# Kernel tuning notes

Measured on AMD Instinct MI355X. Metric: run time of the kernel, lower is better.

Reference implementation:

```python
import jax, jax.numpy as jnp
import numpy as np
from jax import lax

N, C, H, W = 16384, 1, 28, 28
HID = 128
EPS = 1e-5


def setup_inputs() -> dict:
    key = jax.random.key(0)
    ks = jax.random.split(key, 12)
    x = jax.random.normal(ks[0], (N, C, H, W), jnp.float32)
    w1 = jax.random.normal(ks[1], (8, 1, 7, 7), jnp.float32) * 0.05
    g1 = 1.0 + 0.1 * jax.random.normal(ks[2], (8,), jnp.float32)
    b1 = 0.1 * jax.random.normal(ks[3], (8,), jnp.float32)
    w2 = jax.random.normal(ks[4], (10, 8, 5, 5), jnp.float32) * 0.05
    g2 = 1.0 + 0.1 * jax.random.normal(ks[5], (10,), jnp.float32)
    b2 = 0.1 * jax.random.normal(ks[6], (10,), jnp.float32)
    w3 = jax.random.normal(ks[7], (HID, 10, 1, 1), jnp.float32) * 0.05
    g3 = 1.0 + 0.1 * jax.random.normal(ks[8], (HID,), jnp.float32)
    b3 = 0.1 * jax.random.normal(ks[9], (HID,), jnp.float32)
    # original inits fc weight to 0 and bias to identity affine; we add a small
    # random weight so theta varies per sample (exercises the sampler)
    fw = jax.random.normal(ks[10], (6, HID), jnp.float32) * 0.01
    fb = jnp.array([1, 0, 0, 0, 1, 0], jnp.float32)
    return {"x": x, "w1": w1, "g1": g1, "b1": b1, "w2": w2, "g2": g2,
            "b2": b2, "w3": w3, "g3": g3, "b3": b3, "fw": fw, "fb": fb}


def conv2d(x, w):
    return lax.conv_general_dilated(x, w, (1, 1), 'VALID',
                                    dimension_numbers=('NCHW', 'OIHW', 'NCHW'))


def batchnorm(x, g, b):
    m = jnp.mean(x, axis=(0, 2, 3), keepdims=True)
    v = jnp.mean((x - m) ** 2, axis=(0, 2, 3), keepdims=True)
    xh = (x - m) * lax.rsqrt(v + EPS)
    return xh * g[None, :, None, None] + b[None, :, None, None]


def maxpool2(x):
    return lax.reduce_window(x, -jnp.inf, lax.max, (1, 1, 2, 2), (1, 1, 2, 2), 'VALID')


def bilinear_sample(img_nhwc, grid):
    # img_nhwc: [N,H,W,C], grid: [N,H,W,2] normalized coords (x, y) in [-1,1]
    ix = (grid[..., 0] + 1.0) * 0.5 * (W - 1)
    iy = (grid[..., 1] + 1.0) * 0.5 * (H - 1)
    x0f = jnp.floor(ix); y0f = jnp.floor(iy)
    wx = ix - x0f; wy = iy - y0f
    x0 = jnp.clip(x0f.astype(jnp.int32), 0, W - 1)
    x1 = jnp.clip(x0 + 1, 0, W - 1)
    y0 = jnp.clip(y0f.astype(jnp.int32), 0, H - 1)
    y1 = jnp.clip(y0 + 1, 0, H - 1)

    def gather(img, yy, xx):  # img [H,W,C], yy/xx [H,W] -> [H,W,C]
        return img[yy, xx]
    g = jax.vmap(gather)
    v00 = g(img_nhwc, y0, x0)
    v01 = g(img_nhwc, y0, x1)
    v10 = g(img_nhwc, y1, x0)
    v11 = g(img_nhwc, y1, x1)
    wx = wx[..., None]; wy = wy[..., None]
    top = v00 * (1 - wx) + v01 * wx
    bot = v10 * (1 - wx) + v11 * wx
    return top * (1 - wy) + bot * wy


def reference(x, w1, g1, b1, w2, g2, b2, w3, g3, b3, fw, fb):
    # localization network
    xs = jax.nn.relu(maxpool2(batchnorm(conv2d(x, w1), g1, b1)))   # [N,8,11,11]
    xs = jax.nn.relu(maxpool2(batchnorm(conv2d(xs, w2), g2, b2)))  # [N,10,3,3]
    xs = jax.nn.relu(batchnorm(conv2d(xs, w3), g3, b3))            # [N,128,3,3]
    xs = jnp.mean(xs, axis=(2, 3))                                 # avgpool 3x3 -> [N,128]
    theta = (xs @ fw.T + fb).reshape(-1, 2, 3)                     # [N,2,3]
    # affine grid over normalized coords
    lin_x = jnp.linspace(-1.0, 1.0, W)
    lin_y = jnp.linspace(-1.0, 1.0, H)
    gx, gy = jnp.meshgrid(lin_x, lin_y)                            # [H,W]
    base = jnp.stack([gx, gy, jnp.ones_like(gx)], axis=-1)         # [H,W,3]
    grid = jnp.einsum('nij,hwj->nhwi', theta, base)                # [N,H,W,2]
    # sample in NHWC (matches the transpose dance in the torch code)
    out = bilinear_sample(jnp.transpose(x, (0, 2, 3, 1)), grid)
    return jnp.transpose(out, (0, 3, 1, 2))                        # back to NCHW
```

## Files before the change

kernel.cpp:

```cpp
#include <hip/hip_runtime.h>


static constexpr float kEPS = 1e-5f;

#define O_SUM1 0
#define O_SSQ1 8
#define O_SUM2 16
#define O_SSQ2 26
#define O_MOM  36
#define O_W2T  104
#define O_THETA 2112
#define O_E1   100864
#define O_E2   15960576
#define O_E2T  17435136

__global__ __launch_bounds__(256) void k_init(const float* __restrict__ w2,
                                              float* __restrict__ ws){
  int i = blockIdx.x*256 + threadIdx.x;
  if (i < 104) ws[i] = 0.f;
  if (i < 2000){
    int ic = i & 7;
    int r  = i >> 3;
    int kx = r % 5; r /= 5;
    int ky = r % 5; r /= 5;
    int oc = r;
    ws[O_W2T + i] = w2[(oc*8 + ic)*25 + ky*5 + kx];
  }
}

__global__ __launch_bounds__(256) void k_conv1(const float* __restrict__ x,
                                               const float* __restrict__ w1,
                                               const float* __restrict__ g1,
                                               float* __restrict__ ws){
  __shared__ float sw[392];
  const int tid = threadIdx.x;
  for (int i = tid; i < 392; i += 256) sw[i] = w1[i];
  __syncthreads();
  const int gid = blockIdx.x*256 + tid;
  const int ph = gid & 1;
  const int c  = (gid >> 1) & 7;
  const int n  = gid >> 4;
  const float* __restrict__ xs = x + n*784;
  const float* __restrict__ wc = sw + c*49;
  const bool pos = (g1[c] >= 0.f);
  float sum=0.f, ssq=0.f;
  float* __restrict__ outp = ws + O_E1 + n*968 + c;
  const int p0 = ph*6;
  const int p1 = ph ? 11 : 6;
  for (int p=p0; p<p1; p++){
    float cm = 0.f, cn = 0.f;
    #pragma unroll
    for (int h=0; h<2; h++){
      float a0[11], a1[11];
      #pragma unroll
      for (int i=0;i<11;i++){ a0[i]=0.f; a1[i]=0.f; }
      #pragma unroll
      for (int j=0;j<8;j++){
        float in[17];
        const float* __restrict__ rb = xs + (2*p+j)*28 + 11*h;
        if (h==0){
          const float4* __restrict__ rp = (const float4*)rb;
          float4 v0=rp[0], v1=rp[1], v2=rp[2], v3=rp[3];
          in[0]=v0.x; in[1]=v0.y; in[2]=v0.z; in[3]=v0.w;
          in[4]=v1.x; in[5]=v1.y; in[6]=v1.z; in[7]=v1.w;
          in[8]=v2.x; in[9]=v2.y; in[10]=v2.z; in[11]=v2.w;
          in[12]=v3.x; in[13]=v3.y; in[14]=v3.z; in[15]=v3.w;
          in[16]=rb[16];
        } else {
          in[0]=rb[0];
          const float4* __restrict__ rp = (const float4*)(rb+1);
          float4 v0=rp[0], v1=rp[1], v2=rp[2], v3=rp[3];
          in[1]=v0.x; in[2]=v0.y; in[3]=v0.z; in[4]=v0.w;
          in[5]=v1.x; in[6]=v1.y; in[7]=v1.z; in[8]=v1.w;
          in[9]=v2.x; in[10]=v2.y; in[11]=v2.z; in[12]=v2.w;
          in[13]=v3.x; in[14]=v3.y; in[15]=v3.z; in[16]=v3.w;
        }
        if (j < 7){
          #pragma unroll
          for (int kx=0;kx<7;kx++){
            float wv = wc[j*7+kx];
            #pragma unroll
            for (int xo=0;xo<11;xo++) a0[xo] = fmaf(wv, in[xo+kx], a0[xo]);
          }
        }
        if (j >= 1){
          #pragma unroll
          for (int kx=0;kx<7;kx++){
            float wv = wc[(j-1)*7+kx];
            #pragma unroll
            for (int xo=0;xo<11;xo++) a1[xo] = fmaf(wv, in[xo+kx], a1[xo]);
          }
        }
      }
      #pragma unroll
      for (int xo=0;xo<11;xo++){
        sum += a0[xo] + a1[xo];
        ssq = fmaf(a0[xo],a0[xo],ssq);
        ssq = fmaf(a1[xo],a1[xo],ssq);
      }
      if (h==0){
        #pragma unroll
        for (int px=0;px<5;px++){
          float m4 = fmaxf(fmaxf(a0[2*px],a0[2*px+1]), fmaxf(a1[2*px],a1[2*px+1]));
          float n4 = fminf(fminf(a0[2*px],a0[2*px+1]), fminf(a1[2*px],a1[2*px+1]));
          outp[(p*11+px)*8] = pos ? m4 : n4;
        }
        cm = fmaxf(a0[10], a1[10]);
        cn = fminf(a0[10], a1[10]);
      } else {
        float m4 = fmaxf(cm, fmaxf(a0[0],a1[0]));
        float n4 = fminf(cn, fminf(a0[0],a1[0]));
        outp[(p*11+5)*8] = pos ? m4 : n4;
        #pragma unroll
        for (int q=0;q<5;q++){
          int l0 = 1+2*q, l1 = 2+2*q;
          float m4q = fmaxf(fmaxf(a0[l0],a0[l1]), fmaxf(a1[l0],a1[l1]));
          float n4q = fminf(fminf(a0[l0],a0[l1]), fminf(a1[l0],a1[l1]));
          outp[(p*11+6+q)*8] = pos ? m4q : n4q;
        }
      }
    }
  }
  sum += __shfl_xor(sum,1);  ssq += __shfl_xor(ssq,1);
  sum += __shfl_xor(sum,16); ssq += __shfl_xor(ssq,16);
  sum += __shfl_xor(sum,32); ssq += __shfl_xor(ssq,32);
  __shared__ float ls[16];
  if (tid < 16) ls[tid] = 0.f;
  __syncthreads();
  int l = tid & 63;
  if ((l & 0x31) == 0){
    atomicAdd(&ls[l>>1], sum);
    atomicAdd(&ls[8 + (l>>1)], ssq);
  }
  __syncthreads();
  if (tid < 16) atomicAdd(&ws[O_SUM1 + tid], ls[tid]);
}

__global__ __launch_bounds__(256) void k_conv2(float* __restrict__ ws,
                                               const float* __restrict__ g1,
                                               const float* __restrict__ b1,
                                               const float* __restrict__ g2){
  __shared__ float sw2[2160];
  for (int i = threadIdx.x; i < 2000; i += 256){
    int oc_ = i/200, r = i - oc_*200;
    sw2[oc_*216 + r] = ws[O_W2T + i];
  }
  __syncthreads();
  float s1r[8], t1r[8];
  {
    const float invM1 = 1.f/7929856.f;
    #pragma unroll
    for (int c=0;c<8;c++){
      float mean = ws[O_SUM1+c]*invM1;
      float var  = ws[O_SSQ1+c]*invM1 - mean*mean;
      float sc = g1[c]*rsqrtf(var + kEPS);
      s1r[c] = sc; t1r[c] = b1[c] - mean*sc;
    }
  }
  const int blk = blockIdx.x;
  const int half = (blk >= 640) ? 1 : 0;
  const int gid = (blk - half*640)*256 + threadIdx.x;
  const int n = gid/10, oc = gid - 10*n;
  const int r0 = half*4;
  const int nrows = half ? 7 : 8;
  const float* __restrict__ wt = sw2 + oc*216;
  const float* __restrict__ base = ws + O_E1 + n*968;
  float acc[28];
  #pragma unroll
  for (int i=0;i<28;i++) acc[i]=0.f;
  for (int jj=0; jj<nrows; ++jj){
    const int iy = r0 + jj;
    #pragma unroll
    for (int icl=0; icl<2; ++icl){
      float4 in4[11];
      #pragma unroll
      for (int q=0;q<11;q++){
        float4 v = *(const float4*)(base + iy*88 + q*8 + icl*4);
        in4[q].x = fmaxf(fmaf(s1r[icl*4+0], v.x, t1r[icl*4+0]), 0.f);
        in4[q].y = fmaxf(fmaf(s1r[icl*4+1], v.y, t1r[icl*4+1]), 0.f);
        in4[q].z = fmaxf(fmaf(s1r[icl*4+2], v.z, t1r[icl*4+2]), 0.f);
        in4[q].w = fmaxf(fmaf(s1r[icl*4+3], v.w, t1r[icl*4+3]), 0.f);
      }
      #pragma unroll
      for (int ol=0; ol<4; ++ol){
        if (half && ol==3) continue;
        const int ky = jj - ol;
        if (ky < 0 || ky > 4) continue;
        const float* __restrict__ wrow = wt + ky*40 + icl*4;
        #pragma unroll
        for (int kx=0;kx<5;kx++){
          float4 w = *(const float4*)(wrow + kx*8);
          #pragma unroll
          for (int ox=0;ox<7;ox++){
            float a = acc[ol*7+ox];
            a = fmaf(w.x, in4[ox+kx].x, a);
            a = fmaf(w.y, in4[ox+kx].y, a);
            a = fmaf(w.z, in4[ox+kx].z, a);
            a = fmaf(w.w, in4[ox+kx].w, a);
            acc[ol*7+ox] = a;
          }
        }
      }
    }
  }
  {
    const int NV = (half ? 3 : 4)*7;
    float sum=0.f, ssq=0.f;
    #pragma unroll
    for (int i=0;i<28;i++){
      if (i < NV){ float v = acc[i]; sum += v; ssq = fmaf(v,v,ssq); }
    }
    __shared__ float ls[20];
    if (threadIdx.x < 20) ls[threadIdx.x] = 0.f;
    __syncthreads();
    atomicAdd(&ls[oc], sum);
    atomicAdd(&ls[10+oc], ssq);
    __syncthreads();
    if (threadIdx.x < 20) atomicAdd(&ws[O_SUM2 + threadIdx.x], ls[threadIdx.x]);
  }
  {
    const bool pos = (g2[oc] >= 0.f);
    const int npy = half ? 1 : 2;
    #pragma unroll
    for (int pl=0; pl<2; pl++){
      if (pl >= npy) continue;
      const int py = half ? 2 : pl;
      #pragma unroll
      for (int px=0;px<3;px++){
        float v00 = acc[(2*pl)*7   + 2*px], v01 = acc[(2*pl)*7   + 2*px+1];
        float v10 = acc[(2*pl+1)*7 + 2*px], v11 = acc[(2*pl+1)*7 + 2*px+1];
        float m4 = fmaxf(fmaxf(v00,v01), fmaxf(v10,v11));
        float n4 = fminf(fminf(v00,v01), fminf(v10,v11));
        ws[O_E2 + (n*9 + py*3 + px)*10 + oc] = pos ? m4 : n4;
      }
    }
  }
}

__global__ __launch_bounds__(256) void k_pool2fin(float* __restrict__ ws,
                                                  const float* __restrict__ g2,
                                                  const float* __restrict__ b2){
  __shared__ float smom[65];
  const int tid = threadIdx.x;
  if (tid < 65) smom[tid] = 0.f;
  __syncthreads();
  const float invM = 1.f/802816.f;
  const int gid = blockIdx.x*256 + tid;
  const int n = gid/9, p = gid - n*9;
  const float* __restrict__ src = ws + O_E2 + gid*10;
  float xv[10];
  #pragma unroll
  for (int c=0;c<10;c++){
    float mean = ws[O_SUM2+c]*invM;
    float var  = ws[O_SSQ2+c]*invM - mean*mean;
    float sc = g2[c]*rsqrtf(var + kEPS);
    float tc = b2[c] - mean*sc;
    float v = fmaxf(fmaf(sc, src[c], tc), 0.f);
    xv[c] = v;
    ws[O_E2T + (p*10 + c)*16384 + n] = v;
  }
  float mu[10], sm[55];
  #pragma unroll
  for (int i=0;i<10;i++) mu[i] = xv[i];
  #pragma unroll
  for (int i=0;i<10;i++){
    #pragma unroll
    for (int j=i;j<10;j++) sm[i*10 - i*(i-1)/2 + (j-i)] = xv[i]*xv[j];
  }
  #pragma unroll
  for (int off=1; off<64; off<<=1){
    #pragma unroll
    for (int i=0;i<10;i++) mu[i] += __shfl_xor(mu[i], off);
    #pragma unroll
    for (int k=0;k<55;k++) sm[k] += __shfl_xor(sm[k], off);
  }
  if ((tid & 63) == 0){
    #pragma unroll
    for (int i=0;i<10;i++) atomicAdd(&smom[i], mu[i]);
    #pragma unroll
    for (int k=0;k<55;k++) atomicAdd(&smom[10+k], sm[k]);
  }
  __syncthreads();
  if (tid < 65) atomicAdd(&ws[O_MOM + tid], smom[tid]);
}

__global__ __launch_bounds__(64) void k_theta(float* __restrict__ ws,
                                              const float* __restrict__ w3,
                                              const float* __restrict__ g3,
                                              const float* __restrict__ b3,
                                              const float* __restrict__ fw,
                                              const float* __restrict__ fb){
  __shared__ float s3[128], t3[128];
  const int tid = threadIdx.x;
  #pragma unroll
  for (int rep=0; rep<2; rep++){
    const int oc = tid + rep*64;
    const float invM = 1.f/147456.f;
    float mu[10], w[10];
    #pragma unroll
    for (int i=0;i<10;i++) mu[i] = ws[O_MOM+i]*invM;
    #pragma unroll
    for (int i=0;i<10;i++) w[i] = w3[oc*10+i];
    float mean3 = 0.f;
    #pragma unroll
    for (int i=0;i<10;i++) mean3 += w[i]*mu[i];
    float var3 = 0.f;
    #pragma unroll
    for (int i=0;i<10;i++){
      #pragma unroll
      for (int j=i;j<10;j++){
        float Sij = ws[O_MOM+10 + i*10 - i*(i-1)/2 + (j-i)]*invM;
        float cov = Sij - mu[i]*mu[j];
        float coef = (i==j) ? 1.f : 2.f;
        var3 += coef * w[i] * w[j] * cov;
      }
    }
    var3 = fmaxf(var3, 0.f);
    float s = g3[oc]*rsqrtf(var3 + kEPS);
    s3[oc] = s;
    t3[oc] = b3[oc] - mean3*s;
  }
  __syncthreads();
  const int n = blockIdx.x*64 + tid;
  float in[90];
  #pragma unroll
  for (int i=0;i<90;i++) in[i] = ws[O_E2T + i*16384 + n];
  float th[6];
  #pragma unroll
  for (int j=0;j<6;j++) th[j] = fb[j];
  for (int oc=0; oc<128; oc++){
    float s = s3[oc], t = t3[oc];
    float fsum = 0.f;
    #pragma unroll
    for (int p=0;p<9;p++){
      float v = 0.f;
      #pragma unroll
      for (int ic=0;ic<10;ic++) v = fmaf(w3[oc*10+ic], in[p*10+ic], v);
      fsum += fmaxf(fmaf(s,v,t), 0.f);
    }
    float feat = fsum * (1.f/9.f);
    #pragma unroll
    for (int j=0;j<6;j++) th[j] = fmaf(fw[j*128+oc], feat, th[j]);
  }
  float* __restrict__ op = ws + O_THETA + n*6;
  #pragma unroll
  for (int j=0;j<6;j++) op[j] = th[j];
}

__global__ __launch_bounds__(256) void k_sample(const float* __restrict__ x,
                                                const float* __restrict__ ws,
                                                float* __restrict__ out){
  const int n = blockIdx.x;
  __shared__ float sx[784];
  const int tid = threadIdx.x;
  if (tid < 196) ((float4*)sx)[tid] = ((const float4*)(x + n*784))[tid];
  __syncthreads();
  const float* __restrict__ th = ws + O_THETA + n*6;
  const float t0=th[0], t1=th[1], t2=th[2], t3=th[3], t4=th[4], t5=th[5];
  float* __restrict__ op = out + n*784;
  for (int idx=tid; idx<784; idx+=256){
    int h = idx/28;
    int wcol = idx - 28*h;
    float gx = fmaf((float)wcol, 2.f/27.f, -1.f);
    float gy = fmaf((float)h,    2.f/27.f, -1.f);
    float ix = (fmaf(t0,gx,fmaf(t1,gy,t2)) + 1.f)*13.5f;
    float iy = (fmaf(t3,gx,fmaf(t4,gy,t5)) + 1.f)*13.5f;
    float x0f = floorf(ix), y0f = floorf(iy);
    float wx = ix - x0f, wy = iy - y0f;
    int x0 = min(max((int)x0f,0),27); int x1 = min(x0+1,27);
    int y0 = min(max((int)y0f,0),27); int y1 = min(y0+1,27);
    float v00 = sx[y0*28+x0], v01 = sx[y0*28+x1];
    float v10 = sx[y1*28+x0], v11 = sx[y1*28+x1];
    float top = v00*(1.f-wx) + v01*wx;
    float bot = v10*(1.f-wx) + v11*wx;
    op[idx] = top*(1.f-wy) + bot*wy;
  }
}

extern "C" void kernel_launch(void* const* d_in, const int* in_sizes, int n_in,
                              void* d_out, int out_size, void* d_ws, size_t ws_size,
                              hipStream_t stream){
  (void)in_sizes; (void)n_in; (void)out_size; (void)ws_size;
  const float* x  = (const float*)d_in[0];
  const float* w1 = (const float*)d_in[1];
  const float* g1 = (const float*)d_in[2];
  const float* b1 = (const float*)d_in[3];
  const float* w2 = (const float*)d_in[4];
  const float* g2 = (const float*)d_in[5];
  const float* b2 = (const float*)d_in[6];
  const float* w3 = (const float*)d_in[7];
  const float* g3 = (const float*)d_in[8];
  const float* b3 = (const float*)d_in[9];
  const float* fw = (const float*)d_in[10];
  const float* fb = (const float*)d_in[11];
  float* ws  = (float*)d_ws;
  float* out = (float*)d_out;

  hipLaunchKernelGGL(k_init,      dim3(8),     dim3(256), 0, stream, w2, ws);
  hipLaunchKernelGGL(k_conv1,     dim3(1024),  dim3(256), 0, stream, x, w1, g1, ws);
  hipLaunchKernelGGL(k_conv2,     dim3(1280),  dim3(256), 0, stream, ws, g1, b1, g2);
  hipLaunchKernelGGL(k_pool2fin,  dim3(576),   dim3(256), 0, stream, ws, g2, b2);
  hipLaunchKernelGGL(k_theta,     dim3(256),   dim3(64),  0, stream, ws, w3, g3, b3, fw, fb);
  hipLaunchKernelGGL(k_sample,    dim3(16384), dim3(256), 0, stream, x, ws, out);
}
```

Before: 434.7 us.

## Parallelize conv1 across pooled output rows, one thread per row-channel

conv1 threads previously looped over about half of the 11 pooled output rows for a (sample, channel) pair and processed each row in two column halves. Now each thread computes one pooled row across the full 22-column width, and the grid grows from 1024 to 5632 blocks. The aim is more parallelism and latency hiding, and dropping the split-half boundary logic. In exchange each thread holds much larger register arrays (44 accumulators plus 28 inputs), which may lower occupancy, and the 8-row input window is reloaded by overlapping threads rather than streamed.

```diff
diff --git a/kernel.cpp b/kernel.cpp
--- a/kernel.cpp
+++ b/kernel.cpp
@@ -37,100 +37,65 @@
   for (int i = tid; i < 392; i += 256) sw[i] = w1[i];
   __syncthreads();
   const int gid = blockIdx.x*256 + tid;
-  const int ph = gid & 1;
-  const int c  = (gid >> 1) & 7;
-  const int n  = gid >> 4;
+  const int c = gid & 7;
+  const int r = gid >> 3;
+  const int p = r % 11;
+  const int n = r / 11;
   const float* __restrict__ xs = x + n*784;
   const float* __restrict__ wc = sw + c*49;
   const bool pos = (g1[c] >= 0.f);
+  float* __restrict__ outp = ws + O_E1 + n*968 + p*88 + c;
   float sum=0.f, ssq=0.f;
-  float* __restrict__ outp = ws + O_E1 + n*968 + c;
-  const int p0 = ph*6;
-  const int p1 = ph ? 11 : 6;
-  for (int p=p0; p<p1; p++){
-    float cm = 0.f, cn = 0.f;
-    #pragma unroll
-    for (int h=0; h<2; h++){
-      float a0[11], a1[11];
-      #pragma unroll
-      for (int i=0;i<11;i++){ a0[i]=0.f; a1[i]=0.f; }
-      #pragma unroll
-      for (int j=0;j<8;j++){
-        float in[17];
-        const float* __restrict__ rb = xs + (2*p+j)*28 + 11*h;
-        if (h==0){
-          const float4* __restrict__ rp = (const float4*)rb;
-          float4 v0=rp[0], v1=rp[1], v2=rp[2], v3=rp[3];
-          in[0]=v0.x; in[1]=v0.y; in[2]=v0.z; in[3]=v0.w;
-          in[4]=v1.x; in[5]=v1.y; in[6]=v1.z; in[7]=v1.w;
-          in[8]=v2.x; in[9]=v2.y; in[10]=v2.z; in[11]=v2.w;
-          in[12]=v3.x; in[13]=v3.y; in[14]=v3.z; in[15]=v3.w;
-          in[16]=rb[16];
-        } else {
-          in[0]=rb[0];
-          const float4* __restrict__ rp = (const float4*)(rb+1);
-          float4 v0=rp[0], v1=rp[1], v2=rp[2], v3=rp[3];
-          in[1]=v0.x; in[2]=v0.y; in[3]=v0.z; in[4]=v0.w;
-          in[5]=v1.x; in[6]=v1.y; in[7]=v1.z; in[8]=v1.w;
-          in[9]=v2.x; in[10]=v2.y; in[11]=v2.z; in[12]=v2.w;
-          in[13]=v3.x; in[14]=v3.y; in[15]=v3.z; in[16]=v3.w;
-        }
-        if (j < 7){
-          #pragma unroll
-          for (int kx=0;kx<7;kx++){
-            float wv = wc[j*7+kx];
-            #pragma unroll
-            for (int xo=0;xo<11;xo++) a0[xo] = fmaf(wv, in[xo+kx], a0[xo]);
-          }
-        }
-        if (j >= 1){
-          #pragma unroll
-          for (int kx=0;kx<7;kx++){
-            float wv = wc[(j-1)*7+kx];
-            #pragma unroll
-            for (int xo=0;xo<11;xo++) a1[xo] = fmaf(wv, in[xo+kx], a1[xo]);
-          }
-        }
-      }
-      #pragma unroll
-      for (int xo=0;xo<11;xo++){
-        sum += a0[xo] + a1[xo];
-        ssq = fmaf(a0[xo],a0[xo],ssq);
-        ssq = fmaf(a1[xo],a1[xo],ssq);
-      }
-      if (h==0){
+  float a0[22], a1[22];
+  #pragma unroll
+  for (int i=0;i<22;i++){ a0[i]=0.f; a1[i]=0.f; }
+  #pragma unroll
+  for (int j=0;j<8;j++){
+    float in[28];
+    const float4* __restrict__ rp = (const float4*)(xs + (2*p+j)*28);
+    #pragma unroll
+    for (int q=0;q<7;q++){
+      float4 v = rp[q];
+      in[4*q]=v.x; in[4*q+1]=v.y; in[4*q+2]=v.z; in[4*q+3]=v.w;
+    }
+    if (j < 7){
+      #pragma unroll
+      for (int kx=0;kx<7;kx++){
+        float wv = wc[j*7+kx];
         #pragma unroll
-        for (int px=0;px<5;px++){
-          float m4 = fmaxf(fmaxf(a0[2*px],a0[2*px+1]), fmaxf(a1[2*px],a1[2*px+1]));
-          float n4 = fminf(fminf(a0[2*px],a0[2*px+1]), fminf(a1[2*px],a1[2*px+1]));
-          outp[(p*11+px)*8] = pos ? m4 : n4;
-        }
-        cm = fmaxf(a0[10], a1[10]);
-        cn = fminf(a0[10], a1[10]);
-      } else {
-        float m4 = fmaxf(cm, fmaxf(a0[0],a1[0]));
-        float n4 = fminf(cn, fminf(a0[0],a1[0]));
-        outp[(p*11+5)*8] = pos ? m4 : n4;
+        for (int xo=0;xo<22;xo++) a0[xo] = fmaf(wv, in[xo+kx], a0[xo]);
+      }
+    }
+    if (j >= 1){
+      #pragma unroll
+      for (int kx=0;kx<7;kx++){
+        float wv = wc[(j-1)*7+kx];
         #pragma unroll
-        for (int q=0;q<5;q++){
-          int l0 = 1+2*q, l1 = 2+2*q;
-          float m4q = fmaxf(fmaxf(a0[l0],a0[l1]), fmaxf(a1[l0],a1[l1]));
-          float n4q = fminf(fminf(a0[l0],a0[l1]), fminf(a1[l0],a1[l1]));
-          outp[(p*11+6+q)*8] = pos ? m4q : n4q;
-        }
-      }
-    }
-  }
-  sum += __shfl_xor(sum,1);  ssq += __shfl_xor(ssq,1);
+        for (int xo=0;xo<22;xo++) a1[xo] = fmaf(wv, in[xo+kx], a1[xo]);
+      }
+    }
+  }
+  #pragma unroll
+  for (int xo=0;xo<22;xo++){
+    sum += a0[xo] + a1[xo];
+    ssq = fmaf(a0[xo],a0[xo],ssq);
+    ssq = fmaf(a1[xo],a1[xo],ssq);
+  }
+  #pragma unroll
+  for (int px=0;px<11;px++){
+    float m4 = fmaxf(fmaxf(a0[2*px],a0[2*px+1]), fmaxf(a1[2*px],a1[2*px+1]));
+    float n4 = fminf(fminf(a0[2*px],a0[2*px+1]), fminf(a1[2*px],a1[2*px+1]));
+    outp[px*8] = pos ? m4 : n4;
+  }
+  sum += __shfl_xor(sum,8);  ssq += __shfl_xor(ssq,8);
   sum += __shfl_xor(sum,16); ssq += __shfl_xor(ssq,16);
   sum += __shfl_xor(sum,32); ssq += __shfl_xor(ssq,32);
   __shared__ float ls[16];
   if (tid < 16) ls[tid] = 0.f;
   __syncthreads();
-  int l = tid & 63;
-  if ((l & 0x31) == 0){
-    atomicAdd(&ls[l>>1], sum);
-    atomicAdd(&ls[8 + (l>>1)], ssq);
+  if ((tid & 63) < 8){
+    atomicAdd(&ls[tid & 7], sum);
+    atomicAdd(&ls[8 + (tid & 7)], ssq);
   }
   __syncthreads();
   if (tid < 16) atomicAdd(&ws[O_SUM1 + tid], ls[tid]);
@@ -397,7 +362,7 @@
   float* out = (float*)d_out;
 
   hipLaunchKernelGGL(k_init,      dim3(8),     dim3(256), 0, stream, w2, ws);
-  hipLaunchKernelGGL(k_conv1,     dim3(1024),  dim3(256), 0, stream, x, w1, g1, ws);
+  hipLaunchKernelGGL(k_conv1,     dim3(5632),  dim3(256), 0, stream, x, w1, g1, ws);
   hipLaunchKernelGGL(k_conv2,     dim3(1280),  dim3(256), 0, stream, ws, g1, b1, g2);
   hipLaunchKernelGGL(k_pool2fin,  dim3(576),   dim3(256), 0, stream, ws, g2, b2);
   hipLaunchKernelGGL(k_theta,     dim3(256),   dim3(64),  0, stream, ws, w3, g3, b3, fw, fb);
```

After: 376.5 us. 13.4% less time.
